# Kernel tuning notes

Measured on AMD Instinct MI355X. Metric: run time of the kernel, lower is better.

The kernel has to match this reference:

```python
import jax, jax.numpy as jnp
import numpy as np

HS = 2048   # hidden_size
NH = 16     # num_attention_heads
HD = HS // NH  # head_dim = 128
FD = 256    # feature_dim
EPS = 1e-5  # layer_norm_epsilon


def setup_inputs() -> dict:
    key = jax.random.key(0)
    ks = jax.random.split(key, 12)
    s = 0.02
    return {
        "hidden_states": jax.random.normal(ks[0], (2, 4096, HS), jnp.float32),
        "attention_mask": jnp.zeros((2, 4096), jnp.float32),
        "Wq": jax.random.normal(ks[1], (HS, HS), jnp.float32) * s,
        "bq": jnp.zeros((HS,), jnp.float32),
        "Wk": jax.random.normal(ks[2], (HS, HS), jnp.float32) * s,
        "bk": jnp.zeros((HS,), jnp.float32),
        "Wv": jax.random.normal(ks[3], (HS, HS), jnp.float32) * s,
        "bv": jnp.zeros((HS,), jnp.float32),
        "Wo": jax.random.normal(ks[4], (HS, HS), jnp.float32) * s,
        "bo": jnp.zeros((HS,), jnp.float32),
        "Wf1": jax.random.normal(ks[5], (HD, FD), jnp.float32) * s,
        "bf1": jnp.zeros((FD,), jnp.float32),
        "Wf2": jax.random.normal(ks[6], (FD, FD), jnp.float32) * s,
        "bf2": jnp.zeros((FD,), jnp.float32),
        "ln_g": jnp.ones((FD,), jnp.float32),
        "ln_b": jnp.zeros((FD,), jnp.float32),
    }


def reference(hidden_states, attention_mask, Wq, bq, Wk, bk, Wv, bv, Wo, bo,
              Wf1, bf1, Wf2, bf2, ln_g, ln_b):
    B, L, H = hidden_states.shape

    # QKV projections -> [B, NH, L, HD]
    q = (hidden_states @ Wq + bq).reshape(B, L, NH, HD).transpose(0, 2, 1, 3)
    k = (hidden_states @ Wk + bk).reshape(B, L, NH, HD).transpose(0, 2, 1, 3)
    v = (hidden_states @ Wv + bv).reshape(B, L, NH, HD).transpose(0, 2, 1, 3)

    # seq_len (4096) > linear_threshold (1024) -> linear attention branch
    def feature_map(x):  # Linear -> ReLU -> Linear -> LayerNorm
        h = jax.nn.relu(x @ Wf1 + bf1)
        h = h @ Wf2 + bf2
        mu = jnp.mean(h, axis=-1, keepdims=True)
        var = jnp.var(h, axis=-1, keepdims=True)  # biased, like torch LayerNorm
        return (h - mu) * jax.lax.rsqrt(var + EPS) * ln_g + ln_b

    q_feat = feature_map(q)  # [B, NH, L, FD]
    k_feat = feature_map(k)
    # attention_mask [B, L] -> k_feat * (1 + mask)
    k_feat = k_feat * (1.0 + attention_mask[:, None, :, None])

    kv = jnp.einsum('bhlf,bhld->bhfd', k_feat, v)          # [B, NH, FD, HD]
    attn = jnp.einsum('bhlf,bhfd->bhld', q_feat, kv)       # [B, NH, L, HD]
    k_sum = jnp.sum(k_feat, axis=2)                         # [B, NH, FD]
    denom = jnp.einsum('bhlf,bhf->bhl', q_feat, k_sum)[..., None]
    attn = attn / (denom + 1e-8)

    attn = attn.transpose(0, 2, 1, 3).reshape(B, L, H)
    return attn @ Wo + bo
```

## Files before the change

### kernel.cpp

```cpp
#include <hip/hip_runtime.h>

typedef unsigned short u16;
typedef unsigned int u32;
typedef __attribute__((ext_vector_type(8))) short bf16x8;
typedef __attribute__((ext_vector_type(4))) float f32x4;

#define B_ 2
#define L_ 4096
#define HS_ 2048
#define NH_ 16
#define HD_ 128
#define FD_ 256

__device__ __forceinline__ float bf2f(u16 u) { return __uint_as_float(((u32)u) << 16); }
__device__ __forceinline__ u16 f2bf(float f) {
    u32 x = __float_as_uint(f);
    return (u16)((x + 0x7fffu + ((x >> 16) & 1u)) >> 16);
}

__device__ __forceinline__ void llds16(const u16* g, u16* l) {
    __builtin_amdgcn_global_load_lds((const __attribute__((address_space(1))) void*)g,
                                     (__attribute__((address_space(3))) void*)l, 16, 0, 0);
}

__device__ __forceinline__ void gemm_mainloop(const u16* __restrict__ Ab, int lda,
                                              const u16* __restrict__ Bb, int ldb,
                                              int K, u16* As, u16* Bs, f32x4 (&acc)[4][4]) {
    const int tid  = threadIdx.x;
    const int lane = tid & 63;
    const int wave = tid >> 6;
    const int wm = wave >> 1, wn = wave & 1;

    f32x4 zero = {0.f, 0.f, 0.f, 0.f};
#pragma unroll
    for (int i = 0; i < 4; i++)
#pragma unroll
        for (int j = 0; j < 4; j++) acc[i][j] = zero;

    const int srow = lane >> 2;
    const int scol = (lane & 3) * 8;
    const u16* pa = Ab + (size_t)(wave * 32 + srow) * lda + scol;
    const u16* pb = Bb + (size_t)(wave * 32 + srow) * ldb + scol;
    u16* la = As + wave * 1024;
    u16* lb = Bs + wave * 1024;

    const int arow = (wm * 64 + (lane & 15)) * 32 + (lane >> 4) * 8;
    const int brow = (wn * 64 + (lane & 15)) * 32 + (lane >> 4) * 8;

    for (int k0 = 0; k0 < K; k0 += 32) {
        llds16(pa, la);
        llds16(pa + 16 * lda, la + 512);
        llds16(pb, lb);
        llds16(pb + 16 * ldb, lb + 512);
        pa += 32; pb += 32;
        __syncthreads();
        bf16x8 af[4], bg[4];
#pragma unroll
        for (int mt = 0; mt < 4; mt++) af[mt] = *(const bf16x8*)(As + arow + mt * 512);
#pragma unroll
        for (int nt = 0; nt < 4; nt++) bg[nt] = *(const bf16x8*)(Bs + brow + nt * 512);
#pragma unroll
        for (int mt = 0; mt < 4; mt++)
#pragma unroll
            for (int nt = 0; nt < 4; nt++)
                acc[mt][nt] = __builtin_amdgcn_mfma_f32_16x16x32_bf16(af[mt], bg[nt], acc[mt][nt], 0, 0, 0);
        __syncthreads();
    }
}

__global__ __launch_bounds__(256) void k_cvt(const float* __restrict__ src, u16* __restrict__ dst) {
    size_t i = ((size_t)blockIdx.x * 256 + threadIdx.x) * 8;
    float4 a = *(const float4*)(src + i);
    float4 b = *(const float4*)(src + i + 4);
    union { u16 h[8]; uint4 v; } o;
    o.h[0] = f2bf(a.x); o.h[1] = f2bf(a.y); o.h[2] = f2bf(a.z); o.h[3] = f2bf(a.w);
    o.h[4] = f2bf(b.x); o.h[5] = f2bf(b.y); o.h[6] = f2bf(b.z); o.h[7] = f2bf(b.w);
    *(uint4*)(dst + i) = o.v;
}

__global__ __launch_bounds__(256) void k_transpose(const float* Wq, const float* Wk, const float* Wv,
                                                   const float* Wo, const float* Wf1, const float* Wf2,
                                                   u16* Wqkv_t, u16* Wo_t, u16* Wf1_t, u16* Wf2_t) {
    const float* src; u16* dst; int R, C;
    switch (blockIdx.z) {
        case 0: src = Wq;  dst = Wqkv_t;                R = 2048; C = 2048; break;
        case 1: src = Wk;  dst = Wqkv_t + 2048 * 2048;  R = 2048; C = 2048; break;
        case 2: src = Wv;  dst = Wqkv_t + 2 * 2048 * 2048; R = 2048; C = 2048; break;
        case 3: src = Wo;  dst = Wo_t;                  R = 2048; C = 2048; break;
        case 4: src = Wf1; dst = Wf1_t;                 R = 128;  C = 256;  break;
        default: src = Wf2; dst = Wf2_t;                R = 256;  C = 256;  break;
    }
    int c0 = blockIdx.x * 32, r0 = blockIdx.y * 32;
    if (c0 >= C || r0 >= R) return;
    __shared__ u16 tile[32][33];
    int tx = threadIdx.x, ty = threadIdx.y;
    for (int i = ty; i < 32; i += 8) tile[i][tx] = f2bf(src[(size_t)(r0 + i) * C + c0 + tx]);
    __syncthreads();
    for (int i = ty; i < 32; i += 8) dst[(size_t)(c0 + i) * R + r0 + tx] = tile[tx][i];
}

#define QKV_BAR() { __builtin_amdgcn_sched_barrier(0); __builtin_amdgcn_s_barrier(); \
                    __builtin_amdgcn_sched_barrier(0); }
#define QKV_LGKM0() { asm volatile("s_waitcnt lgkmcnt(0)" ::: "memory"); \
                      __builtin_amdgcn_sched_barrier(0); }

__global__ __launch_bounds__(512, 2) void k_gemm_qkv(
        const u16* __restrict__ X, const u16* __restrict__ Wt,
        const float* __restrict__ bq, const float* __restrict__ bk, const float* __restrict__ bv,
        u16* __restrict__ qout, u16* __restrict__ kout, u16* __restrict__ vT) {
    __shared__ u16 LDS[65536];
    const int tid = threadIdx.x, lane = tid & 63, wave = tid >> 6;
    const int wm = wave >> 2, wn = wave & 3;

    const int xcd = blockIdx.x & 7, idx = blockIdx.x >> 3;
    const int nblk = idx >> 2;
    const int mblk = xcd * 4 + (idx & 3);
    const int mb = mblk * 256, nb = nblk * 256;

    int r0g, c0g, r1g, c1g;
    { int p = tid * 16; int s = p >> 10, q = p & 1023; q ^= ((q >> 9) & 1) << 5;
      r0g = (s >> 1) * 16 + (q >> 6); c0g = (s & 1) * 32 + ((q & 63) >> 1); }
    { int p = 8192 + tid * 16; int s = p >> 10, q = p & 1023; q ^= ((q >> 9) & 1) << 5;
      r1g = (s >> 1) * 16 + (q >> 6); c1g = (s & 1) * 32 + ((q & 63) >> 1); }
    const int voff0 = r0g * HS_ + c0g;
    const int voff1 = r1g * HS_ + c1g;

    int qby = (lane & 15) * 64 + (lane >> 4) * 16;
    qby ^= ((qby >> 9) & 1) << 5;
    const int qh = qby >> 1;

#define STG(G, soff, dstu) { \
    llds16((G) + (soff) + voff0, LDS + (dstu) + wave * 512); \
    llds16((G) + (soff) + voff1, LDS + (dstu) + 4096 + wave * 512); }

    const size_t a0 = (size_t)mb * HS_, a1 = (size_t)(mb + 128) * HS_;
    const size_t b0 = (size_t)nb * HS_, b1 = (size_t)(nb + 128) * HS_;

    STG(Wt, b0, 32768); STG(Wt, b1, 40960);
    STG(X,  a0, 0);     STG(X,  a1, 8192);
    STG(Wt, b0 + 64, 49152); STG(Wt, b1 + 64, 57344);
    STG(X,  a0 + 64, 16384);
    asm volatile("s_waitcnt vmcnt(6)" ::: "memory");
    QKV_BAR();

    f32x4 acc[8][4];
    f32x4 zero = {0.f, 0.f, 0.f, 0.f};
#pragma unroll
    for (int i = 0; i < 8; i++)
#pragma unroll
        for (int j = 0; j < 4; j++) acc[i][j] = zero;

    const int NT = HS_ / 64;
    bf16x8 afr[4][2], bfr[4][2];
    for (int t = 0; t < NT; t++) {
        const int bsel = t & 1;
        const u16* Ah = LDS + bsel * 16384 + wm * 8192;
        const u16* Bh = LDS + 32768 + bsel * 16384 + (wn >> 1) * 8192;
        const int bg0 = (wn & 1) * 4;
        const size_t kc1 = (size_t)(t + 1) * 64, kc2 = (size_t)(t + 2) * 64;

#pragma unroll
        for (int mf = 0; mf < 4; mf++)
#pragma unroll
            for (int ks = 0; ks < 2; ks++)
                afr[mf][ks] = *(const bf16x8*)(Ah + (mf * 2 + ks) * 512 + qh);
#pragma unroll
        for (int nf = 0; nf < 4; nf++)
#pragma unroll
            for (int ks = 0; ks < 2; ks++)
                bfr[nf][ks] = *(const bf16x8*)(Bh + ((bg0 + nf) * 2 + ks) * 512 + qh);
        if (t + 1 < NT) STG(X, a1 + kc1, (bsel ^ 1) * 16384 + 8192);
        QKV_BAR();
        QKV_LGKM0();
        __builtin_amdgcn_s_setprio(1);
#pragma unroll
        for (int mf = 0; mf < 4; mf++)
#pragma unroll
            for (int nf = 0; nf < 2; nf++)
#pragma unroll
                for (int ks = 0; ks < 2; ks++)
                    acc[mf][nf] = __builtin_amdgcn_mfma_f32_16x16x32_bf16(afr[mf][ks], bfr[nf][ks], acc[mf][nf], 0, 0, 0);
        __builtin_amdgcn_s_setprio(0);
        QKV_BAR();
        if (t + 2 < NT) STG(Wt, b0 + kc2, 32768 + bsel * 16384);
        QKV_BAR();
        __builtin_amdgcn_s_setprio(1);
#pragma unroll
        for (int mf = 0; mf < 4; mf++)
#pragma unroll
            for (int nf = 2; nf < 4; nf++)
#pragma unroll
                for (int ks = 0; ks < 2; ks++)
                    acc[mf][nf] = __builtin_amdgcn_mfma_f32_16x16x32_bf16(afr[mf][ks], bfr[nf][ks], acc[mf][nf], 0, 0, 0);
        __builtin_amdgcn_s_setprio(0);
        QKV_BAR();
#pragma unroll
        for (int mf = 0; mf < 4; mf++)
#pragma unroll
            for (int ks = 0; ks < 2; ks++)
                afr[mf][ks] = *(const bf16x8*)(Ah + ((mf + 4) * 2 + ks) * 512 + qh);
        if (t + 2 < NT) STG(Wt, b1 + kc2, 32768 + bsel * 16384 + 8192);
        QKV_BAR();
        QKV_LGKM0();
        __builtin_amdgcn_s_setprio(1);
#pragma unroll
        for (int mf = 0; mf < 4; mf++)
#pragma unroll
            for (int nf = 0; nf < 2; nf++)
#pragma unroll
                for (int ks = 0; ks < 2; ks++)
                    acc[mf + 4][nf] = __builtin_amdgcn_mfma_f32_16x16x32_bf16(afr[mf][ks], bfr[nf][ks], acc[mf + 4][nf], 0, 0, 0);
        __builtin_amdgcn_s_setprio(0);
        QKV_BAR();
        if (t + 2 < NT) STG(X, a0 + kc2, bsel * 16384);
        QKV_BAR();
        __builtin_amdgcn_s_setprio(1);
#pragma unroll
        for (int mf = 0; mf < 4; mf++)
#pragma unroll
            for (int nf = 2; nf < 4; nf++)
#pragma unroll
                for (int ks = 0; ks < 2; ks++)
                    acc[mf + 4][nf] = __builtin_amdgcn_mfma_f32_16x16x32_bf16(afr[mf][ks], bfr[nf][ks], acc[mf + 4][nf], 0, 0, 0);
        __builtin_amdgcn_s_setprio(0);
        if (t + 2 < NT) { asm volatile("s_waitcnt vmcnt(6)" ::: "memory"); }
        else if (t + 1 < NT) { asm volatile("s_waitcnt vmcnt(0)" ::: "memory"); }
        QKV_BAR();
    }
#undef STG

    const int which = nblk >> 3;
    const int colbase = (nblk & 7) * 256;
    const int bi = mb >> 12, lb = mb & 4095;
    const float* bias = (which == 0) ? bq : (which == 1 ? bk : bv);
    const int rb = (lane >> 4) << 2, cl = lane & 15;

    if (which < 2) {
        u16* dst = (which == 0) ? qout : kout;
        const int bh0 = bi * NH_ + (colbase >> 7);
        for (int half = 0; half < 2; half++) {
            if (wm == half) {
#pragma unroll
                for (int nf = 0; nf < 4; nf++) {
                    float bvv = bias[colbase + wn * 64 + nf * 16 + cl];
#pragma unroll
                    for (int mf = 0; mf < 8; mf++)
#pragma unroll
                        for (int r = 0; r < 4; r++)
                            LDS[(mf * 16 + rb + r) * 264 + wn * 64 + nf * 16 + cl] =
                                f2bf(acc[mf][nf][r] + bvv);
                }
            }
            __syncthreads();
#pragma unroll
            for (int it = 0; it < 8; it++) {
                int row = (tid >> 5) + it * 16;
                int c8 = (tid & 31) * 8;
                uint2 lo = *(const uint2*)(LDS + row * 264 + c8);
                uint2 hi = *(const uint2*)(LDS + row * 264 + c8 + 4);
                uint4 val = make_uint4(lo.x, lo.y, hi.x, hi.y);
                u16* pp = dst + ((size_t)(bh0 + (c8 >> 7)) * L_ + lb + half * 128 + row) * HD_ + (c8 & 127);
                *(uint4*)pp = val;
            }
            __syncthreads();
        }
    } else {
        for (int half = 0; half < 2; half++) {
            if (wm == half) {
#pragma unroll
                for (int nf = 0; nf < 4; nf++) {
                    float bvv = bias[colbase + wn * 64 + nf * 16 + cl];
#pragma unroll
                    for (int mf = 0; mf < 8; mf++)
#pragma unroll
                        for (int r = 0; r < 4; r++)
                            LDS[(wn * 64 + nf * 16 + cl) * 136 + mf * 16 + rb + r] =
                                f2bf(acc[mf][nf][r] + bvv);
                }
            }
            __syncthreads();
#pragma unroll
            for (int it = 0; it < 8; it++) {
                int n = (tid >> 4) + it * 32;
                int c8 = (tid & 15) * 8;
                uint2 lo = *(const uint2*)(LDS + n * 136 + c8);
                uint2 hi = *(const uint2*)(LDS + n * 136 + c8 + 4);
                uint4 val = make_uint4(lo.x, lo.y, hi.x, hi.y);
                int cg = colbase + n;
                u16* pp = vT + ((size_t)(bi * NH_ + (cg >> 7)) * HD_ + (cg & 127)) * L_ + lb + half * 128 + c8;
                *(uint4*)pp = val;
            }
            __syncthreads();
        }
    }
}

template <int MASKED, int TRANS>
__global__ __launch_bounds__(256) void k_feat(const u16* __restrict__ X,
                                              const u16* __restrict__ W1t, const float* __restrict__ b1,
                                              const u16* __restrict__ W2t, const float* __restrict__ b2,
                                              const float* __restrict__ g, const float* __restrict__ be,
                                              const float* __restrict__ mask,
                                              u16* __restrict__ feat, float* __restrict__ ksp) {
    __shared__ u16 As[64 * 32];
    __shared__ u16 Bs[256 * 32];
    __shared__ u16 H[64 * 264];
    __shared__ float MU[64], RS[64], FAC[64];
    const int tid = threadIdx.x, lane = tid & 63, wave = tid >> 6;
    const int mb = blockIdx.x * 64;

    const int srow = lane >> 2, scol = (lane & 3) * 8;
    const int arow_rd = (lane & 15);
    const int kgrp = (lane >> 4) * 8;

    f32x4 acc[4][4];
    f32x4 zero = {0.f, 0.f, 0.f, 0.f};
#pragma unroll
    for (int i = 0; i < 4; i++)
#pragma unroll
        for (int j = 0; j < 4; j++) acc[i][j] = zero;

    for (int k0 = 0; k0 < 128; k0 += 32) {
        llds16(X + (size_t)(mb + wave * 16 + srow) * 128 + k0 + scol, As + wave * 512);
#pragma unroll
        for (int i = 0; i < 4; i++)
            llds16(W1t + (size_t)((wave * 4 + i) * 16 + srow) * 128 + k0 + scol,
                   Bs + (wave * 4 + i) * 512);
        __syncthreads();
        bf16x8 af[4], bg[4];
#pragma unroll
        for (int mt = 0; mt < 4; mt++) af[mt] = *(const bf16x8*)(As + (mt * 16 + arow_rd) * 32 + kgrp);
#pragma unroll
        for (int nt = 0; nt < 4; nt++) bg[nt] = *(const bf16x8*)(Bs + (wave * 64 + nt * 16 + arow_rd) * 32 + kgrp);
#pragma unroll
        for (int mt = 0; mt < 4; mt++)
#pragma unroll
            for (int nt = 0; nt < 4; nt++)
                acc[mt][nt] = __builtin_amdgcn_mfma_f32_16x16x32_bf16(af[mt], bg[nt], acc[mt][nt], 0, 0, 0);
        __syncthreads();
    }
    {
        const int rbase = (lane >> 4) << 2;
#pragma unroll
        for (int nt = 0; nt < 4; nt++) {
            int n = wave * 64 + nt * 16 + (lane & 15);
            float bvv = b1[n];
#pragma unroll
            for (int mt = 0; mt < 4; mt++)
#pragma unroll
                for (int r = 0; r < 4; r++) {
                    float v = fmaxf(acc[mt][nt][r] + bvv, 0.f);
                    H[(mt * 16 + rbase + r) * 264 + n] = f2bf(v);
                }
            acc[0][nt] = zero; acc[1][nt] = zero; acc[2][nt] = zero; acc[3][nt] = zero;
        }
    }
    __syncthreads();

    for (int k0 = 0; k0 < 256; k0 += 32) {
#pragma unroll
        for (int i = 0; i < 4; i++)
            llds16(W2t + (size_t)((wave * 4 + i) * 16 + srow) * 256 + k0 + scol,
                   Bs + (wave * 4 + i) * 512);
        __syncthreads();
        bf16x8 af[4], bg[4];
#pragma unroll
        for (int mt = 0; mt < 4; mt++) af[mt] = *(const bf16x8*)(H + (mt * 16 + arow_rd) * 264 + k0 + kgrp);
#pragma unroll
        for (int nt = 0; nt < 4; nt++) bg[nt] = *(const bf16x8*)(Bs + (wave * 64 + nt * 16 + arow_rd) * 32 + kgrp);
#pragma unroll
        for (int mt = 0; mt < 4; mt++)
#pragma unroll
            for (int nt = 0; nt < 4; nt++)
                acc[mt][nt] = __builtin_amdgcn_mfma_f32_16x16x32_bf16(af[mt], bg[nt], acc[mt][nt], 0, 0, 0);
        __syncthreads();
    }
    {
        const int rbase = (lane >> 4) << 2;
#pragma unroll
        for (int nt = 0; nt < 4; nt++) {
            int n = wave * 64 + nt * 16 + (lane & 15);
            float bvv = b2[n];
#pragma unroll
            for (int mt = 0; mt < 4; mt++)
#pragma unroll
                for (int r = 0; r < 4; r++)
                    H[(mt * 16 + rbase + r) * 264 + n] = f2bf(acc[mt][nt][r] + bvv);
        }
    }
    __syncthreads();

    {
        for (int r = 0; r < 16; r++) {
            int row = wave * 16 + r;
            int j = lane * 4;
            uint2 u = *(const uint2*)(H + row * 264 + j);
            float x0 = bf2f((u16)(u.x & 0xffff)), x1 = bf2f((u16)(u.x >> 16));
            float x2 = bf2f((u16)(u.y & 0xffff)), x3 = bf2f((u16)(u.y >> 16));
            float s = x0 + x1 + x2 + x3;
            float ss = x0 * x0 + x1 * x1 + x2 * x2 + x3 * x3;
#pragma unroll
            for (int o = 32; o >= 1; o >>= 1) { s += __shfl_xor(s, o); ss += __shfl_xor(ss, o); }
            if (lane == 0) {
                float mu = s * (1.f / FD_);
                float var = ss * (1.f / FD_) - mu * mu;
                MU[row] = mu;
                RS[row] = rsqrtf(var + 1e-5f);
                float fac = 1.f;
                if (MASKED) {
                    int grow = mb + row;
                    int b = grow >> 16;
                    int l = grow & 4095;
                    fac = 1.f + mask[b * L_ + l];
                }
                FAC[row] = fac;
            }
        }
    }
    __syncthreads();

    if (!TRANS) {
        int j = lane * 4;
        float4 gg = *(const float4*)(g + j);
        float4 bb = *(const float4*)(be + j);
        for (int r = 0; r < 16; r++) {
            int row = wave * 16 + r;
            float mu = MU[row], rstd = RS[row], fac = FAC[row];
            uint2 u = *(const uint2*)(H + row * 264 + j);
            float x0 = bf2f((u16)(u.x & 0xffff)), x1 = bf2f((u16)(u.x >> 16));
            float x2 = bf2f((u16)(u.y & 0xffff)), x3 = bf2f((u16)(u.y >> 16));
            uint2 o2;
            o2.x = (u32)f2bf(((x0 - mu) * rstd * gg.x + bb.x) * fac) |
                   ((u32)f2bf(((x1 - mu) * rstd * gg.y + bb.y) * fac) << 16);
            o2.y = (u32)f2bf(((x2 - mu) * rstd * gg.z + bb.z) * fac) |
                   ((u32)f2bf(((x3 - mu) * rstd * gg.w + bb.w) * fac) << 16);
            *(uint2*)(feat + (size_t)(mb + row) * FD_ + j) = o2;
        }
    } else {
        int f = tid;
        int bh = mb >> 12, lb = mb & 4095;
        float gf = g[f], bf = be[f];
        u16* orow = feat + ((size_t)bh * FD_ + f) * L_ + lb;
        float fsum = 0.f;
        for (int lg = 0; lg < 64; lg += 8) {
            union { u16 h8[8]; uint4 v4; } pk;
#pragma unroll
            for (int j = 0; j < 8; j++) {
                int row = lg + j;
                float x = bf2f(H[row * 264 + f]);
                float y = ((x - MU[row]) * RS[row] * gf + bf) * FAC[row];
                fsum += y;
                pk.h8[j] = f2bf(y);
            }
            *(uint4*)(orow + lg) = pk.v4;
        }
        ksp[((size_t)bh * 64 + (lb >> 6)) * FD_ + f] = fsum;
    }
}

__global__ __launch_bounds__(256) void k_ksum2(const float* __restrict__ ksp, float* __restrict__ ksum) {
    const int bh = blockIdx.x, f = threadIdx.x;
    float s = 0.f;
    for (int i = 0; i < 64; i++) s += ksp[((size_t)bh * 64 + i) * FD_ + f];
    ksum[(size_t)bh * FD_ + f] = s;
}

__global__ __launch_bounds__(256) void k_gemm_kv(const u16* __restrict__ kfT, const u16* __restrict__ vT,
                                                 float* __restrict__ kvp) {
    __shared__ u16 As[4096], Bs[4096];
    f32x4 acc[4][4];
    const int mb = blockIdx.x * 128;
    const int ks = blockIdx.y;
    const int bh = blockIdx.z;
    gemm_mainloop(kfT + ((size_t)bh * FD_ + mb) * L_ + ks * 512, L_,
                  vT + (size_t)bh * HD_ * L_ + ks * 512, L_, 512, As, Bs, acc);
    const int lane = threadIdx.x & 63, wave = threadIdx.x >> 6;
    const int wm = wave >> 1, wn = wave & 1;
    const int n0 = wn * 64 + (lane & 15);
    const int m0 = mb + wm * 64 + ((lane >> 4) << 2);
    float* o = kvp + (size_t)(ks * 32 + bh) * (FD_ * HD_);
#pragma unroll
    for (int nt = 0; nt < 4; nt++)
#pragma unroll
        for (int mt = 0; mt < 4; mt++)
#pragma unroll
            for (int r = 0; r < 4; r++)
                o[(size_t)(m0 + mt * 16 + r) * HD_ + n0 + nt * 16] = acc[mt][nt][r];
}

__global__ __launch_bounds__(256) void k_kvred(const float* __restrict__ kvp, u16* __restrict__ kvT) {
    const int p = blockIdx.x, bh = blockIdx.y, t = threadIdx.x;
    const int e0 = p * 4096 + t * 16;
    float s[16];
#pragma unroll
    for (int i = 0; i < 16; i++) s[i] = 0.f;
    for (int c = 0; c < 8; c++) {
        const float* src = kvp + ((size_t)(c * 32 + bh)) * 32768 + e0;
#pragma unroll
        for (int i = 0; i < 16; i += 4) {
            float4 vv = *(const float4*)(src + i);
            s[i] += vv.x; s[i + 1] += vv.y; s[i + 2] += vv.z; s[i + 3] += vv.w;
        }
    }
#pragma unroll
    for (int i = 0; i < 16; i++) {
        int e = e0 + i, fq = e >> 7, d = e & 127;
        kvT[((size_t)bh * HD_ + d) * FD_ + fq] = f2bf(s[i]);
    }
}

__global__ __launch_bounds__(256) void k_denom(const u16* __restrict__ qf, const float* __restrict__ ksum,
                                               float* __restrict__ denom) {
    const int lane = threadIdx.x & 63, wave = threadIdx.x >> 6;
    const size_t row = (size_t)blockIdx.x * 4 + wave;
    const int bh = (int)(row >> 12);
    uint2 u = *(const uint2*)(qf + row * FD_ + lane * 4);
    float4 kk = *(const float4*)(ksum + (size_t)bh * FD_ + lane * 4);
    float d = bf2f((u16)(u.x & 0xffff)) * kk.x + bf2f((u16)(u.x >> 16)) * kk.y
            + bf2f((u16)(u.y & 0xffff)) * kk.z + bf2f((u16)(u.y >> 16)) * kk.w;
#pragma unroll
    for (int o = 32; o >= 1; o >>= 1) d += __shfl_xor(d, o);
    if (lane == 0) denom[row] = d;
}

__global__ __launch_bounds__(256) void k_gemm_attn(const u16* __restrict__ qf, const u16* __restrict__ kvT,
                                                   const float* __restrict__ denom, u16* __restrict__ attn) {
    __shared__ u16 S[128 * 132];
    f32x4 acc[4][4];
    const int mb = blockIdx.x * 128;
    const int bh = blockIdx.y;
    gemm_mainloop(qf + ((size_t)bh * L_ + mb) * FD_, FD_, kvT + (size_t)bh * HD_ * FD_, FD_, FD_, S, S + 4096, acc);
    const int tid = threadIdx.x, lane = tid & 63, wave = tid >> 6;
    const int wm = wave >> 1, wn = wave & 1;
    const int b = bh >> 4, h = bh & 15;
    const int mloc = wm * 64 + ((lane >> 4) << 2);
    const int nloc = wn * 64 + (lane & 15);
#pragma unroll
    for (int mt = 0; mt < 4; mt++)
#pragma unroll
        for (int r = 0; r < 4; r++) {
            int l = mb + mloc + mt * 16 + r;
            float rden = 1.f / (denom[(size_t)bh * L_ + l] + 1e-8f);
#pragma unroll
            for (int nt = 0; nt < 4; nt++)
                S[(mloc + mt * 16 + r) * 132 + nloc + nt * 16] = f2bf(acc[mt][nt][r] * rden);
        }
    __syncthreads();
    const int c8 = (tid & 15) * 8;
#pragma unroll
    for (int it = 0; it < 8; it++) {
        int row = (tid >> 4) + it * 16;
        uint2 lo = *(const uint2*)(S + row * 132 + c8);
        uint2 hi = *(const uint2*)(S + row * 132 + c8 + 4);
        uint4 val = make_uint4(lo.x, lo.y, hi.x, hi.y);
        *(uint4*)(attn + ((size_t)(b * L_ + mb + row)) * HS_ + h * HD_ + c8) = val;
    }
}

__global__ __launch_bounds__(256) void k_gemm_out(const u16* __restrict__ A, const u16* __restrict__ Wt,
                                                  const float* __restrict__ bo, float* __restrict__ out) {
    __shared__ u16 As[4096], Bs[4096];
    f32x4 acc[4][4];
    const int bid = blockIdx.y * 64 + blockIdx.x;
    const int mblk = (bid / 128) * 8 + (bid & 7);
    const int nblk = (bid >> 3) % 16;
    const int mb = mblk * 128, nb = nblk * 128;
    gemm_mainloop(A + (size_t)mb * HS_, HS_, Wt + (size_t)nb * HS_, HS_, HS_, As, Bs, acc);
    const int lane = threadIdx.x & 63, wave = threadIdx.x >> 6;
    const int wm = wave >> 1, wn = wave & 1;
    const int n0 = nb + wn * 64 + (lane & 15);
    const int m0 = mb + wm * 64 + ((lane >> 4) << 2);
#pragma unroll
    for (int nt = 0; nt < 4; nt++) {
        int n = n0 + nt * 16;
        float bvv = bo[n];
#pragma unroll
        for (int mt = 0; mt < 4; mt++)
#pragma unroll
            for (int r = 0; r < 4; r++)
                out[(size_t)(m0 + mt * 16 + r) * HS_ + n] = acc[mt][nt][r] + bvv;
    }
}

extern "C" void kernel_launch(void* const* d_in, const int* in_sizes, int n_in,
                              void* d_out, int out_size, void* d_ws, size_t ws_size,
                              hipStream_t stream) {
    const float* hs  = (const float*)d_in[0];
    const float* msk = (const float*)d_in[1];
    const float* Wq  = (const float*)d_in[2];  const float* bq  = (const float*)d_in[3];
    const float* Wk  = (const float*)d_in[4];  const float* bk  = (const float*)d_in[5];
    const float* Wv  = (const float*)d_in[6];  const float* bv  = (const float*)d_in[7];
    const float* Wo  = (const float*)d_in[8];  const float* bo  = (const float*)d_in[9];
    const float* Wf1 = (const float*)d_in[10]; const float* bf1 = (const float*)d_in[11];
    const float* Wf2 = (const float*)d_in[12]; const float* bf2 = (const float*)d_in[13];
    const float* lng = (const float*)d_in[14]; const float* lnb = (const float*)d_in[15];
    float* out = (float*)d_out;
    char* w = (char*)d_ws;

    u16* qfeat  = (u16*)(w + 0);
    u16* Wqkv_t = (u16*)(w + 0);
    u16* Xbf    = (u16*)(w + 25165824u);
    u16* kfT    = (u16*)(w + 67108864u);
    u16* qbuf   = (u16*)(w + 134217728u);
    float* kvp  = (float*)(w + 134217728u);
    u16* kbuf   = (u16*)(w + 167772160u);
    u16* attn   = (u16*)(w + 167772160u);
    u16* vT     = (u16*)(w + 201326592u);
    u16* Wo_t   = (u16*)(w + 234881024u);
    u16* Wf1_t  = (u16*)(w + 243269632u);
    u16* Wf2_t  = (u16*)(w + 243335168u);
    float* ksp  = (float*)(w + 243466240u);
    u16* kvT    = (u16*)(w + 245563392u);
    float* ksum = (float*)(w + 247660544u);
    float* denom = (float*)(w + 247693312u);

    k_cvt<<<dim3(8192), 256, 0, stream>>>(hs, Xbf);
    k_transpose<<<dim3(64, 64, 6), dim3(32, 8), 0, stream>>>(Wq, Wk, Wv, Wo, Wf1, Wf2,
                                                             Wqkv_t, Wo_t, Wf1_t, Wf2_t);
    k_gemm_qkv<<<dim3(768), 512, 0, stream>>>(Xbf, Wqkv_t, bq, bk, bv, qbuf, kbuf, vT);
    k_feat<0, 0><<<dim3(2048), 256, 0, stream>>>(qbuf, Wf1_t, bf1, Wf2_t, bf2, lng, lnb, msk, qfeat, ksp);
    k_feat<1, 1><<<dim3(2048), 256, 0, stream>>>(kbuf, Wf1_t, bf1, Wf2_t, bf2, lng, lnb, msk, kfT, ksp);
    k_ksum2<<<dim3(32), 256, 0, stream>>>(ksp, ksum);
    k_gemm_kv<<<dim3(2, 8, 32), 256, 0, stream>>>(kfT, vT, kvp);
    k_kvred<<<dim3(8, 32), 256, 0, stream>>>(kvp, kvT);
    k_denom<<<dim3(32768), 256, 0, stream>>>(qfeat, ksum, denom);
    k_gemm_attn<<<dim3(32, 32), 256, 0, stream>>>(qfeat, kvT, denom, attn);
    k_gemm_out<<<dim3(64, 16), 256, 0, stream>>>(attn, Wo_t, bo, out);
}
```

Before: 717.0 us.

## Reuse tuned 256x256 QKV GEMM mainloop for output projection; batch denom rows

Factors the pipelined 256x256-tile, 512-thread mainloop out of the QKV GEMM into a shared device function. The output projection GEMM now uses it in place of the older 128x128 tile loop, giving more reuse per LDS load and the tuned prefetch schedule. Separately, the denominator kernel now has each wave handle four rows and loads the ksum vector once, cutting block count by four. The out GEMM grid drops to 256 blocks, which is fewer than two waves of work per CU on a large GPU, so occupancy and tail balance may change.

```diff
diff --git a/kernel.cpp b/kernel.cpp
--- a/kernel.cpp
+++ b/kernel.cpp
@@ -104,18 +104,11 @@
 #define QKV_LGKM0() { asm volatile("s_waitcnt lgkmcnt(0)" ::: "memory"); \
                       __builtin_amdgcn_sched_barrier(0); }
 
-__global__ __launch_bounds__(512, 2) void k_gemm_qkv(
-        const u16* __restrict__ X, const u16* __restrict__ Wt,
-        const float* __restrict__ bq, const float* __restrict__ bk, const float* __restrict__ bv,
-        u16* __restrict__ qout, u16* __restrict__ kout, u16* __restrict__ vT) {
-    __shared__ u16 LDS[65536];
+__device__ __forceinline__ void mainloop256(const u16* __restrict__ Abase,
+                                            const u16* __restrict__ Bbase,
+                                            u16* LDS, f32x4 (&acc)[8][4]) {
     const int tid = threadIdx.x, lane = tid & 63, wave = tid >> 6;
     const int wm = wave >> 2, wn = wave & 3;
-
-    const int xcd = blockIdx.x & 7, idx = blockIdx.x >> 3;
-    const int nblk = idx >> 2;
-    const int mblk = xcd * 4 + (idx & 3);
-    const int mb = mblk * 256, nb = nblk * 256;
 
     int r0g, c0g, r1g, c1g;
     { int p = tid * 16; int s = p >> 10, q = p & 1023; q ^= ((q >> 9) & 1) << 5;
@@ -133,17 +126,16 @@
     llds16((G) + (soff) + voff0, LDS + (dstu) + wave * 512); \
     llds16((G) + (soff) + voff1, LDS + (dstu) + 4096 + wave * 512); }
 
-    const size_t a0 = (size_t)mb * HS_, a1 = (size_t)(mb + 128) * HS_;
-    const size_t b0 = (size_t)nb * HS_, b1 = (size_t)(nb + 128) * HS_;
-
-    STG(Wt, b0, 32768); STG(Wt, b1, 40960);
-    STG(X,  a0, 0);     STG(X,  a1, 8192);
-    STG(Wt, b0 + 64, 49152); STG(Wt, b1 + 64, 57344);
-    STG(X,  a0 + 64, 16384);
+    const size_t a0 = 0, a1 = (size_t)128 * HS_;
+    const size_t b0 = 0, b1 = (size_t)128 * HS_;
+
+    STG(Bbase, b0, 32768); STG(Bbase, b1, 40960);
+    STG(Abase, a0, 0);     STG(Abase, a1, 8192);
+    STG(Bbase, b0 + 64, 49152); STG(Bbase, b1 + 64, 57344);
+    STG(Abase, a0 + 64, 16384);
     asm volatile("s_waitcnt vmcnt(6)" ::: "memory");
     QKV_BAR();
 
-    f32x4 acc[8][4];
     f32x4 zero = {0.f, 0.f, 0.f, 0.f};
 #pragma unroll
     for (int i = 0; i < 8; i++)
@@ -169,7 +161,7 @@
 #pragma unroll
             for (int ks = 0; ks < 2; ks++)
                 bfr[nf][ks] = *(const bf16x8*)(Bh + ((bg0 + nf) * 2 + ks) * 512 + qh);
-        if (t + 1 < NT) STG(X, a1 + kc1, (bsel ^ 1) * 16384 + 8192);
+        if (t + 1 < NT) STG(Abase, a1 + kc1, (bsel ^ 1) * 16384 + 8192);
         QKV_BAR();
         QKV_LGKM0();
         __builtin_amdgcn_s_setprio(1);
@@ -182,7 +174,7 @@
                     acc[mf][nf] = __builtin_amdgcn_mfma_f32_16x16x32_bf16(afr[mf][ks], bfr[nf][ks], acc[mf][nf], 0, 0, 0);
         __builtin_amdgcn_s_setprio(0);
         QKV_BAR();
-        if (t + 2 < NT) STG(Wt, b0 + kc2, 32768 + bsel * 16384);
+        if (t + 2 < NT) STG(Bbase, b0 + kc2, 32768 + bsel * 16384);
         QKV_BAR();
         __builtin_amdgcn_s_setprio(1);
 #pragma unroll
@@ -199,7 +191,7 @@
 #pragma unroll
             for (int ks = 0; ks < 2; ks++)
                 afr[mf][ks] = *(const bf16x8*)(Ah + ((mf + 4) * 2 + ks) * 512 + qh);
-        if (t + 2 < NT) STG(Wt, b1 + kc2, 32768 + bsel * 16384 + 8192);
+        if (t + 2 < NT) STG(Bbase, b1 + kc2, 32768 + bsel * 16384 + 8192);
         QKV_BAR();
         QKV_LGKM0();
         __builtin_amdgcn_s_setprio(1);
@@ -212,7 +204,7 @@
                     acc[mf + 4][nf] = __builtin_amdgcn_mfma_f32_16x16x32_bf16(afr[mf][ks], bfr[nf][ks], acc[mf + 4][nf], 0, 0, 0);
         __builtin_amdgcn_s_setprio(0);
         QKV_BAR();
-        if (t + 2 < NT) STG(X, a0 + kc2, bsel * 16384);
+        if (t + 2 < NT) STG(Abase, a0 + kc2, bsel * 16384);
         QKV_BAR();
         __builtin_amdgcn_s_setprio(1);
 #pragma unroll
@@ -228,6 +220,23 @@
         QKV_BAR();
     }
 #undef STG
+}
+
+__global__ __launch_bounds__(512, 2) void k_gemm_qkv(
+        const u16* __restrict__ X, const u16* __restrict__ Wt,
+        const float* __restrict__ bq, const float* __restrict__ bk, const float* __restrict__ bv,
+        u16* __restrict__ qout, u16* __restrict__ kout, u16* __restrict__ vT) {
+    __shared__ u16 LDS[65536];
+    const int tid = threadIdx.x, lane = tid & 63, wave = tid >> 6;
+    const int wm = wave >> 2, wn = wave & 3;
+
+    const int xcd = blockIdx.x & 7, idx = blockIdx.x >> 3;
+    const int nblk = idx >> 2;
+    const int mblk = xcd * 4 + (idx & 3);
+    const int mb = mblk * 256, nb = nblk * 256;
+
+    f32x4 acc[8][4];
+    mainloop256(X + (size_t)mb * HS_, Wt + (size_t)nb * HS_, LDS, acc);
 
     const int which = nblk >> 3;
     const int colbase = (nblk & 7) * 256;
@@ -291,6 +300,35 @@
                 *(uint4*)pp = val;
             }
             __syncthreads();
+        }
+    }
+}
+
+__global__ __launch_bounds__(512, 2) void k_gemm_out(const u16* __restrict__ A, const u16* __restrict__ Wt,
+                                                     const float* __restrict__ bo, float* __restrict__ out) {
+    __shared__ u16 LDS[65536];
+    const int lane = threadIdx.x & 63, wave = threadIdx.x >> 6;
+    const int wm = wave >> 2, wn = wave & 3;
+
+    const int xcd = blockIdx.x & 7, idx = blockIdx.x >> 3;
+    const int nblk = idx >> 2;
+    const int mblk = xcd * 4 + (idx & 3);
+    const int mb = mblk * 256, nb = nblk * 256;
+
+    f32x4 acc[8][4];
+    mainloop256(A + (size_t)mb * HS_, Wt + (size_t)nb * HS_, LDS, acc);
+
+    const int rb = (lane >> 4) << 2, cl = lane & 15;
+#pragma unroll
+    for (int nf = 0; nf < 4; nf++) {
+        int n = nb + wn * 64 + nf * 16 + cl;
+        float bvv = bo[n];
+#pragma unroll
+        for (int mf = 0; mf < 8; mf++) {
+            int m = mb + wm * 128 + mf * 16 + rb;
+#pragma unroll
+            for (int r = 0; r < 4; r++)
+                out[(size_t)(m + r) * HS_ + n] = acc[mf][nf][r] + bvv;
         }
     }
 }
@@ -512,15 +550,19 @@
 __global__ __launch_bounds__(256) void k_denom(const u16* __restrict__ qf, const float* __restrict__ ksum,
                                                float* __restrict__ denom) {
     const int lane = threadIdx.x & 63, wave = threadIdx.x >> 6;
-    const size_t row = (size_t)blockIdx.x * 4 + wave;
-    const int bh = (int)(row >> 12);
-    uint2 u = *(const uint2*)(qf + row * FD_ + lane * 4);
+    const size_t row0 = (size_t)blockIdx.x * 16 + wave * 4;
+    const int bh = (int)(row0 >> 12);
     float4 kk = *(const float4*)(ksum + (size_t)bh * FD_ + lane * 4);
-    float d = bf2f((u16)(u.x & 0xffff)) * kk.x + bf2f((u16)(u.x >> 16)) * kk.y
-            + bf2f((u16)(u.y & 0xffff)) * kk.z + bf2f((u16)(u.y >> 16)) * kk.w;
-#pragma unroll
-    for (int o = 32; o >= 1; o >>= 1) d += __shfl_xor(d, o);
-    if (lane == 0) denom[row] = d;
+#pragma unroll
+    for (int rr = 0; rr < 4; rr++) {
+        size_t row = row0 + rr;
+        uint2 u = *(const uint2*)(qf + row * FD_ + lane * 4);
+        float d = bf2f((u16)(u.x & 0xffff)) * kk.x + bf2f((u16)(u.x >> 16)) * kk.y
+                + bf2f((u16)(u.y & 0xffff)) * kk.z + bf2f((u16)(u.y >> 16)) * kk.w;
+#pragma unroll
+        for (int o = 32; o >= 1; o >>= 1) d += __shfl_xor(d, o);
+        if (lane == 0) denom[row] = d;
+    }
 }
 
 __global__ __launch_bounds__(256) void k_gemm_attn(const u16* __restrict__ qf, const u16* __restrict__ kvT,
@@ -554,31 +596,6 @@
         uint2 hi = *(const uint2*)(S + row * 132 + c8 + 4);
         uint4 val = make_uint4(lo.x, lo.y, hi.x, hi.y);
         *(uint4*)(attn + ((size_t)(b * L_ + mb + row)) * HS_ + h * HD_ + c8) = val;
-    }
-}
-
-__global__ __launch_bounds__(256) void k_gemm_out(const u16* __restrict__ A, const u16* __restrict__ Wt,
-                                                  const float* __restrict__ bo, float* __restrict__ out) {
-    __shared__ u16 As[4096], Bs[4096];
-    f32x4 acc[4][4];
-    const int bid = blockIdx.y * 64 + blockIdx.x;
-    const int mblk = (bid / 128) * 8 + (bid & 7);
-    const int nblk = (bid >> 3) % 16;
-    const int mb = mblk * 128, nb = nblk * 128;
-    gemm_mainloop(A + (size_t)mb * HS_, HS_, Wt + (size_t)nb * HS_, HS_, HS_, As, Bs, acc);
-    const int lane = threadIdx.x & 63, wave = threadIdx.x >> 6;
-    const int wm = wave >> 1, wn = wave & 1;
-    const int n0 = nb + wn * 64 + (lane & 15);
-    const int m0 = mb + wm * 64 + ((lane >> 4) << 2);
-#pragma unroll
-    for (int nt = 0; nt < 4; nt++) {
-        int n = n0 + nt * 16;
-        float bvv = bo[n];
-#pragma unroll
-        for (int mt = 0; mt < 4; mt++)
-#pragma unroll
-            for (int r = 0; r < 4; r++)
-                out[(size_t)(m0 + mt * 16 + r) * HS_ + n] = acc[mt][nt][r] + bvv;
     }
 }
 
@@ -623,7 +640,7 @@
     k_ksum2<<<dim3(32), 256, 0, stream>>>(ksp, ksum);
     k_gemm_kv<<<dim3(2, 8, 32), 256, 0, stream>>>(kfT, vT, kvp);
     k_kvred<<<dim3(8, 32), 256, 0, stream>>>(kvp, kvT);
-    k_denom<<<dim3(32768), 256, 0, stream>>>(qfeat, ksum, denom);
+    k_denom<<<dim3(8192), 256, 0, stream>>>(qfeat, ksum, denom);
     k_gemm_attn<<<dim3(32, 32), 256, 0, stream>>>(qfeat, kvT, denom, attn);
-    k_gemm_out<<<dim3(64, 16), 256, 0, stream>>>(attn, Wo_t, bo, out);
-}
+    k_gemm_out<<<dim3(256), 512, 0, stream>>>(attn, Wo_t, bo, out);
+}
```

Measured after the change: 699.0 us. -2.5%, faster.
